# Kernel optimization log

Measured on AMD Instinct MI355X. Metric: run time of the kernel, lower is better.

## Reference

```python
import jax, jax.numpy as jnp
import numpy as np

K = 20  # number of top neighbors kept per row
NOISE_SCALE = 1e-4


def setup_inputs() -> dict:
    key = jax.random.key(0)
    k1, k2 = jax.random.split(key)
    B, N = 16, 2048
    A = jax.random.normal(k1, (B, N, N), dtype=jnp.float32)
    noise = jax.random.uniform(k2, (B, N, N), dtype=jnp.float32)
    return {"A": A, "noise": noise}


def reference(A, noise):
    # _activate: ReLU
    A = jax.nn.relu(A)

    # _sparsify: per-row top-k on noise-doped scores, scatter a 0/1 mask, multiply
    A_doped = A + noise * NOISE_SCALE
    _, topk_idx = jax.lax.top_k(A_doped, K)  # (B, N, K)
    B, N, _ = A.shape
    b_idx = jnp.arange(B)[:, None, None]
    r_idx = jnp.arange(N)[None, :, None]
    mask = jnp.zeros_like(A).at[b_idx, r_idx, topk_idx].set(1.0)
    A = A * mask

    # _symmetrize
    A = (A + jnp.swapaxes(A, 1, 2)) * 0.5

    # _normalize ('sym'): A <- D^{-1/2} (A + I) D^{-1/2}
    A = A + jnp.eye(N, dtype=A.dtype)
    d_inv = jnp.sum(A, axis=2) ** -0.5  # (B, N)
    d_inv = jnp.where(jnp.isinf(d_inv), 0.0, d_inv)
    # diag(d) @ A @ diag(d) expressed via broadcasting (same math as batched matmul)
    A = d_inv[:, :, None] * A * d_inv[:, None, :]
    return A
```

## Files before the change

### kernel.cpp

```cpp
#include <hip/hip_runtime.h>

#define NN 2048
#define KK 20
#define BB 16

__global__ __launch_bounds__(256) void topk_kernel(
    const float* __restrict__ A, const float* __restrict__ noise,
    int* __restrict__ sel_idx, float* __restrict__ sel_val,
    float* __restrict__ colsum)
{
    __shared__ int tie_idx[4][64];
    __shared__ int tie_cnt[4];

    const int lane = threadIdx.x & 63;
    const int wv   = threadIdx.x >> 6;
    const int row  = blockIdx.x * 4 + wv;
    const float* Ar = A     + (size_t)row * NN;
    const float* Nr = noise + (size_t)row * NN;

    float key[32];
#pragma unroll
    for (int c = 0; c < 8; ++c) {
        float4 a4 = *(const float4*)(Ar + c * 256 + lane * 4);
        float4 n4 = *(const float4*)(Nr + c * 256 + lane * 4);
        key[c*4+0] = fmaxf(a4.x, 0.f) + n4.x * 1e-4f;
        key[c*4+1] = fmaxf(a4.y, 0.f) + n4.y * 1e-4f;
        key[c*4+2] = fmaxf(a4.z, 0.f) + n4.z * 1e-4f;
        key[c*4+3] = fmaxf(a4.w, 0.f) + n4.w * 1e-4f;
    }

    unsigned lo = 0u, hi = 0x7F800000u;
    unsigned tb = 0u;
    bool exact = false;
    while (hi - lo > 1u) {
        unsigned mid = (lo + hi) >> 1;
        float tm = __uint_as_float(mid);
        int c = 0;
#pragma unroll
        for (int j = 0; j < 32; ++j)
            c += __popcll(__ballot(key[j] >= tm));
        if (c == KK) { tb = mid; exact = true; break; }
        if (c > KK) lo = mid; else hi = mid;
    }

    const unsigned long long ltm = (1ull << lane) - 1ull;
    const int colbase = row & ~(NN - 1);
    int*   si = sel_idx + (size_t)row * KK;
    float* sv = sel_val + (size_t)row * KK;

    if (exact) {
        float t = __uint_as_float(tb);
        int run = 0;
#pragma unroll
        for (int j = 0; j < 32; ++j) {
            bool p = key[j] >= t;
            unsigned long long m = __ballot(p);
            if (p) {
                int pos = run + __popcll(m & ltm);
                int idx = (j >> 2) * 256 + lane * 4 + (j & 3);
                float v = fmaxf(Ar[idx], 0.f);
                si[pos] = idx; sv[pos] = v;
                atomicAdd(&colsum[colbase + idx], v);
            }
            run += __popcll(m);
        }
    } else {
        float t1 = __uint_as_float(lo);
        int run = 0;
#pragma unroll
        for (int j = 0; j < 32; ++j) {
            bool p = key[j] > t1;
            unsigned long long m = __ballot(p);
            if (p) {
                int pos = run + __popcll(m & ltm);
                int idx = (j >> 2) * 256 + lane * 4 + (j & 3);
                float v = fmaxf(Ar[idx], 0.f);
                si[pos] = idx; sv[pos] = v;
                atomicAdd(&colsum[colbase + idx], v);
            }
            run += __popcll(m);
        }
        if (lane == 0) tie_cnt[wv] = 0;
#pragma unroll
        for (int j = 0; j < 32; ++j) {
            if (key[j] == t1) {
                int p = atomicAdd(&tie_cnt[wv], 1);
                if (p < 64) tie_idx[wv][p] = (j >> 2) * 256 + lane * 4 + (j & 3);
            }
        }
        if (lane == 0) {
            int n = tie_cnt[wv]; if (n > 64) n = 64;
            int need = KK - run;
            for (int s = 0; s < need; ++s) {
                int bq = 0, bidx = 0x7fffffff;
                for (int q = 0; q < n; ++q) {
                    int v = tie_idx[wv][q];
                    if (v < bidx) { bidx = v; bq = q; }
                }
                tie_idx[wv][bq] = 0x7fffffff;
                float v = fmaxf(Ar[bidx], 0.f);
                si[run + s] = bidx; sv[run + s] = v;
                atomicAdd(&colsum[colbase + bidx], v);
            }
        }
    }
}

__global__ __launch_bounds__(256) void dinv_kernel(
    const float* __restrict__ sel_val, const float* __restrict__ colsum,
    float* __restrict__ dinv, float* __restrict__ out)
{
    int r = blockIdx.x * 256 + threadIdx.x;
    const float* sv = sel_val + (size_t)r * KK;
    float rs = 0.f;
#pragma unroll
    for (int k = 0; k < KK; ++k) rs += sv[k];
    float d  = 1.0f + 0.5f * (rs + colsum[r]);
    float dv = 1.0f / sqrtf(d);
    dinv[r] = dv;
    int b = r >> 11, i = r & (NN - 1);
    out[((size_t)b << 22) + ((size_t)i << 11) + i] = dv * dv;
}

__global__ __launch_bounds__(256) void scatter_kernel(
    const int* __restrict__ sel_idx, const float* __restrict__ sel_val,
    const float* __restrict__ dinv, float* __restrict__ out)
{
    int t = blockIdx.x * 256 + threadIdx.x;
    int r = t / KK;
    int k = t - r * KK;
    int b = r >> 11, i = r & (NN - 1);
    int j = sel_idx[(size_t)r * KK + k];
    float v = sel_val[(size_t)r * KK + k];
    float c = 0.5f * v * dinv[r] * dinv[(r & ~(NN - 1)) + j];
    size_t base = (size_t)b << 22;
    atomicAdd(out + base + ((size_t)i << 11) + j, c);
    atomicAdd(out + base + ((size_t)j << 11) + i, c);
}

extern "C" void kernel_launch(void* const* d_in, const int* in_sizes, int n_in,
                              void* d_out, int out_size, void* d_ws, size_t ws_size,
                              hipStream_t stream)
{
    const float* A     = (const float*)d_in[0];
    const float* noise = (const float*)d_in[1];
    float* out = (float*)d_out;
    char*  ws  = (char*)d_ws;

    const int rows = BB * NN;
    int*   sel_idx = (int*)ws;
    float* sel_val = (float*)(ws + 2621440);
    float* colsum  = (float*)(ws + 5242880);
    float* dinv    = (float*)(ws + 5242880 + 131072);

    hipMemsetAsync(colsum, 0, rows * sizeof(float), stream);
    hipMemsetAsync(out, 0, (size_t)out_size * sizeof(float), stream);

    topk_kernel<<<rows / 4, 256, 0, stream>>>(A, noise, sel_idx, sel_val, colsum);
    dinv_kernel<<<rows / 256, 256, 0, stream>>>(sel_val, colsum, dinv, out);
    scatter_kernel<<<rows * KK / 256, 256, 0, stream>>>(sel_idx, sel_val, dinv, out);
}
```

Measured before the change: 686.8 us.

## Prefilter top-k candidates by fixed threshold and build output rows densely in LDS

The top-k kernel now handles two rows per wavefront and keeps only elements above a fixed threshold (1.8) as candidates in LDS. The bisection search then runs over at most 128 candidates, with a full-row fallback when the count is out of range. The output is no longer memset and then filled by global atomics; each row is assembled in shared memory from its own edges plus a per-column reverse list, then written once with coalesced stores. The fixed threshold relies on the input distribution (standard normal) to keep the candidate count in range, and the reverse list caps each column at 64 entries.

```diff
diff --git a/kernel.cpp b/kernel.cpp
--- a/kernel.cpp
+++ b/kernel.cpp
@@ -3,139 +3,275 @@
 #define NN 2048
 #define KK 20
 #define BB 16
+#define ROWS (BB * NN)
+#define T0F 1.8f
+#define CAP 128
+#define CSLOT 64
+
+__device__ __forceinline__ float wred(float x) {
+#pragma unroll
+    for (int s = 32; s; s >>= 1) x += __shfl_xor(x, s);
+    return x;
+}
 
 __global__ __launch_bounds__(256) void topk_kernel(
     const float* __restrict__ A, const float* __restrict__ noise,
     int* __restrict__ sel_idx, float* __restrict__ sel_val,
-    float* __restrict__ colsum)
-{
-    __shared__ int tie_idx[4][64];
-    __shared__ int tie_cnt[4];
+    float* __restrict__ rowsum)
+{
+    __shared__ float cand_key[8][CAP];
+    __shared__ int   cand_idx[8][CAP];
+    __shared__ int   tie_buf[4][64];
+    __shared__ int   tie_n[4];
 
     const int lane = threadIdx.x & 63;
     const int wv   = threadIdx.x >> 6;
-    const int row  = blockIdx.x * 4 + wv;
-    const float* Ar = A     + (size_t)row * NN;
-    const float* Nr = noise + (size_t)row * NN;
-
-    float key[32];
+    const int row0 = blockIdx.x * 8 + wv * 2;
+    const unsigned long long ltm = (1ull << lane) - 1ull;
+
+    const float* Ap[2] = { A + (size_t)row0 * NN, A + (size_t)(row0 + 1) * NN };
+    const float* Np[2] = { noise + (size_t)row0 * NN, noise + (size_t)(row0 + 1) * NN };
+
+    int cnt[2] = {0, 0};
 #pragma unroll
     for (int c = 0; c < 8; ++c) {
-        float4 a4 = *(const float4*)(Ar + c * 256 + lane * 4);
-        float4 n4 = *(const float4*)(Nr + c * 256 + lane * 4);
-        key[c*4+0] = fmaxf(a4.x, 0.f) + n4.x * 1e-4f;
-        key[c*4+1] = fmaxf(a4.y, 0.f) + n4.y * 1e-4f;
-        key[c*4+2] = fmaxf(a4.z, 0.f) + n4.z * 1e-4f;
-        key[c*4+3] = fmaxf(a4.w, 0.f) + n4.w * 1e-4f;
-    }
-
-    unsigned lo = 0u, hi = 0x7F800000u;
-    unsigned tb = 0u;
-    bool exact = false;
-    while (hi - lo > 1u) {
-        unsigned mid = (lo + hi) >> 1;
-        float tm = __uint_as_float(mid);
-        int c = 0;
-#pragma unroll
-        for (int j = 0; j < 32; ++j)
-            c += __popcll(__ballot(key[j] >= tm));
-        if (c == KK) { tb = mid; exact = true; break; }
-        if (c > KK) lo = mid; else hi = mid;
-    }
-
-    const unsigned long long ltm = (1ull << lane) - 1ull;
-    const int colbase = row & ~(NN - 1);
-    int*   si = sel_idx + (size_t)row * KK;
-    float* sv = sel_val + (size_t)row * KK;
-
-    if (exact) {
-        float t = __uint_as_float(tb);
-        int run = 0;
-#pragma unroll
-        for (int j = 0; j < 32; ++j) {
-            bool p = key[j] >= t;
+#pragma unroll
+        for (int rr = 0; rr < 2; ++rr) {
+            float4 a4 = *(const float4*)(Ap[rr] + c * 256 + lane * 4);
+            float4 n4 = *(const float4*)(Np[rr] + c * 256 + lane * 4);
+            float kk4[4] = { fmaxf(a4.x, 0.f) + n4.x * 1e-4f,
+                             fmaxf(a4.y, 0.f) + n4.y * 1e-4f,
+                             fmaxf(a4.z, 0.f) + n4.z * 1e-4f,
+                             fmaxf(a4.w, 0.f) + n4.w * 1e-4f };
+#pragma unroll
+            for (int e = 0; e < 4; ++e) {
+                bool p = kk4[e] >= T0F;
+                unsigned long long m = __ballot(p);
+                if (p) {
+                    int pos = cnt[rr] + __popcll(m & ltm);
+                    if (pos < CAP) {
+                        cand_key[wv * 2 + rr][pos] = kk4[e];
+                        cand_idx[wv * 2 + rr][pos] = c * 256 + lane * 4 + e;
+                    }
+                }
+                cnt[rr] += __popcll(m);
+            }
+        }
+    }
+
+    float c0[2], c1[2];
+#pragma unroll
+    for (int rr = 0; rr < 2; ++rr) {
+        c0[rr] = (lane      < cnt[rr] && lane      < CAP) ? cand_key[wv*2+rr][lane]      : -1.f;
+        c1[rr] = (lane + 64 < cnt[rr] && lane + 64 < CAP) ? cand_key[wv*2+rr][lane + 64] : -1.f;
+    }
+    unsigned lo[2], hi[2], tb[2] = {0, 0};
+    int act[2], ex[2] = {0, 0};
+#pragma unroll
+    for (int rr = 0; rr < 2; ++rr) {
+        act[rr] = (cnt[rr] > KK && cnt[rr] <= CAP);
+        lo[rr] = __float_as_uint(T0F);
+        float mx = fmaxf(c0[rr], c1[rr]);
+#pragma unroll
+        for (int s = 32; s; s >>= 1) mx = fmaxf(mx, __shfl_xor(mx, s));
+        hi[rr] = __float_as_uint(fmaxf(mx, T0F)) + 1u;
+    }
+    while (act[0] | act[1]) {
+#pragma unroll
+        for (int rr = 0; rr < 2; ++rr) {
+            if (act[rr]) {
+                unsigned mid = (lo[rr] + hi[rr]) >> 1;
+                float tm = __uint_as_float(mid);
+                int c = __popcll(__ballot(c0[rr] >= tm)) +
+                        __popcll(__ballot(c1[rr] >= tm));
+                if (c == KK) { tb[rr] = mid; ex[rr] = 1; act[rr] = 0; }
+                else {
+                    if (c > KK) lo[rr] = mid; else hi[rr] = mid;
+                    if (hi[rr] - lo[rr] <= 1u) act[rr] = 0;
+                }
+            }
+        }
+    }
+
+#pragma unroll
+    for (int rr = 0; rr < 2; ++rr) {
+        const int row = row0 + rr;
+        int*   si = sel_idx + (size_t)row * KK;
+        float* sv = sel_val + (size_t)row * KK;
+        float acc = 0.f;
+        if (cnt[rr] == KK) {
+            if (lane < KK) {
+                int idx = cand_idx[wv * 2 + rr][lane];
+                float v = fmaxf(Ap[rr][idx], 0.f);
+                si[lane] = idx; sv[lane] = v; acc = v;
+            }
+            float rs = wred(acc);
+            if (lane == 0) rowsum[row] = rs;
+        } else if (ex[rr]) {
+            float t = __uint_as_float(tb[rr]);
+            bool p = c0[rr] >= t;
             unsigned long long m = __ballot(p);
             if (p) {
-                int pos = run + __popcll(m & ltm);
-                int idx = (j >> 2) * 256 + lane * 4 + (j & 3);
-                float v = fmaxf(Ar[idx], 0.f);
-                si[pos] = idx; sv[pos] = v;
-                atomicAdd(&colsum[colbase + idx], v);
-            }
-            run += __popcll(m);
-        }
-    } else {
-        float t1 = __uint_as_float(lo);
-        int run = 0;
-#pragma unroll
-        for (int j = 0; j < 32; ++j) {
-            bool p = key[j] > t1;
-            unsigned long long m = __ballot(p);
+                int pos = __popcll(m & ltm);
+                int idx = cand_idx[wv * 2 + rr][lane];
+                float v = fmaxf(Ap[rr][idx], 0.f);
+                si[pos] = idx; sv[pos] = v; acc += v;
+            }
+            int run = __popcll(m);
+            p = c1[rr] >= t;
+            m = __ballot(p);
             if (p) {
                 int pos = run + __popcll(m & ltm);
-                int idx = (j >> 2) * 256 + lane * 4 + (j & 3);
-                float v = fmaxf(Ar[idx], 0.f);
-                si[pos] = idx; sv[pos] = v;
-                atomicAdd(&colsum[colbase + idx], v);
-            }
-            run += __popcll(m);
+                int idx = cand_idx[wv * 2 + rr][lane + 64];
+                float v = fmaxf(Ap[rr][idx], 0.f);
+                si[pos] = idx; sv[pos] = v; acc += v;
+            }
+            float rs = wred(acc);
+            if (lane == 0) rowsum[row] = rs;
+        } else {
+            unsigned flo = 0u, fhi = 0x7F800000u, ftb = 0u;
+            int fex = 0;
+            while (fhi - flo > 1u) {
+                unsigned mid = (flo + fhi) >> 1;
+                float tm = __uint_as_float(mid);
+                int c = 0;
+                for (int j = 0; j < 32; ++j) {
+                    int idx = j * 64 + lane;
+                    float k = fmaxf(Ap[rr][idx], 0.f) + Np[rr][idx] * 1e-4f;
+                    c += __popcll(__ballot(k >= tm));
+                }
+                if (c == KK) { ftb = mid; fex = 1; break; }
+                if (c > KK) flo = mid; else fhi = mid;
+            }
+            if (fex) {
+                float t = __uint_as_float(ftb);
+                int run = 0;
+                for (int j = 0; j < 32; ++j) {
+                    int idx = j * 64 + lane;
+                    float v = fmaxf(Ap[rr][idx], 0.f);
+                    bool p = (v + Np[rr][idx] * 1e-4f) >= t;
+                    unsigned long long m = __ballot(p);
+                    if (p) {
+                        int pos = run + __popcll(m & ltm);
+                        si[pos] = idx; sv[pos] = v; acc += v;
+                    }
+                    run += __popcll(m);
+                }
+                float rs = wred(acc);
+                if (lane == 0) rowsum[row] = rs;
+            } else {
+                float t1 = __uint_as_float(flo);
+                int run = 0;
+                for (int j = 0; j < 32; ++j) {
+                    int idx = j * 64 + lane;
+                    float v = fmaxf(Ap[rr][idx], 0.f);
+                    bool p = (v + Np[rr][idx] * 1e-4f) > t1;
+                    unsigned long long m = __ballot(p);
+                    if (p) {
+                        int pos = run + __popcll(m & ltm);
+                        si[pos] = idx; sv[pos] = v; acc += v;
+                    }
+                    run += __popcll(m);
+                }
+                if (lane == 0) tie_n[wv] = 0;
+                for (int j = 0; j < 32; ++j) {
+                    int idx = j * 64 + lane;
+                    float k = fmaxf(Ap[rr][idx], 0.f) + Np[rr][idx] * 1e-4f;
+                    if (k == t1) {
+                        int p = atomicAdd(&tie_n[wv], 1);
+                        if (p < 64) tie_buf[wv][p] = idx;
+                    }
+                }
+                float rs = wred(acc);
+                if (lane == 0) {
+                    int n = tie_n[wv]; if (n > 64) n = 64;
+                    int need = KK - run;
+                    float extra = 0.f;
+                    for (int s = 0; s < need; ++s) {
+                        int bq = 0, bidx = 0x7fffffff;
+                        for (int q = 0; q < n; ++q)
+                            if (tie_buf[wv][q] < bidx) { bidx = tie_buf[wv][q]; bq = q; }
+                        tie_buf[wv][bq] = 0x7fffffff;
+                        float v = fmaxf(Ap[rr][bidx], 0.f);
+                        si[run + s] = bidx; sv[run + s] = v; extra += v;
+                    }
+                    rowsum[row] = rs + extra;
+                }
+            }
         }
-        if (lane == 0) tie_cnt[wv] = 0;
-#pragma unroll
-        for (int j = 0; j < 32; ++j) {
-            if (key[j] == t1) {
-                int p = atomicAdd(&tie_cnt[wv], 1);
-                if (p < 64) tie_idx[wv][p] = (j >> 2) * 256 + lane * 4 + (j & 3);
-            }
-        }
-        if (lane == 0) {
-            int n = tie_cnt[wv]; if (n > 64) n = 64;
-            int need = KK - run;
-            for (int s = 0; s < need; ++s) {
-                int bq = 0, bidx = 0x7fffffff;
-                for (int q = 0; q < n; ++q) {
-                    int v = tie_idx[wv][q];
-                    if (v < bidx) { bidx = v; bq = q; }
-                }
-                tie_idx[wv][bq] = 0x7fffffff;
-                float v = fmaxf(Ar[bidx], 0.f);
-                si[run + s] = bidx; sv[run + s] = v;
-                atomicAdd(&colsum[colbase + bidx], v);
-            }
-        }
-    }
+    }
+}
+
+__global__ __launch_bounds__(256) void colsum_kernel(
+    const int* __restrict__ sel_idx, const float* __restrict__ sel_val,
+    float* __restrict__ colsum)
+{
+    int t = blockIdx.x * 256 + threadIdx.x;
+    int r = t / KK;
+    int cb = r & ~(NN - 1);
+    atomicAdd(&colsum[cb + sel_idx[t]], sel_val[t]);
 }
 
 __global__ __launch_bounds__(256) void dinv_kernel(
-    const float* __restrict__ sel_val, const float* __restrict__ colsum,
-    float* __restrict__ dinv, float* __restrict__ out)
+    const float* __restrict__ rowsum, const float* __restrict__ colsum,
+    float* __restrict__ dinv, float* __restrict__ diag2)
 {
     int r = blockIdx.x * 256 + threadIdx.x;
-    const float* sv = sel_val + (size_t)r * KK;
-    float rs = 0.f;
-#pragma unroll
-    for (int k = 0; k < KK; ++k) rs += sv[k];
-    float d  = 1.0f + 0.5f * (rs + colsum[r]);
+    float d = 1.0f + 0.5f * (rowsum[r] + colsum[r]);
     float dv = 1.0f / sqrtf(d);
     dinv[r] = dv;
-    int b = r >> 11, i = r & (NN - 1);
-    out[((size_t)b << 22) + ((size_t)i << 11) + i] = dv * dv;
-}
-
-__global__ __launch_bounds__(256) void scatter_kernel(
+    diag2[r] = dv * dv;
+}
+
+__global__ __launch_bounds__(256) void edge_kernel(
     const int* __restrict__ sel_idx, const float* __restrict__ sel_val,
-    const float* __restrict__ dinv, float* __restrict__ out)
+    const float* __restrict__ dinv, float* __restrict__ out_val,
+    int* __restrict__ col_cnt, unsigned short* __restrict__ col_pack)
 {
     int t = blockIdx.x * 256 + threadIdx.x;
     int r = t / KK;
     int k = t - r * KK;
-    int b = r >> 11, i = r & (NN - 1);
-    int j = sel_idx[(size_t)r * KK + k];
-    float v = sel_val[(size_t)r * KK + k];
-    float c = 0.5f * v * dinv[r] * dinv[(r & ~(NN - 1)) + j];
-    size_t base = (size_t)b << 22;
-    atomicAdd(out + base + ((size_t)i << 11) + j, c);
-    atomicAdd(out + base + ((size_t)j << 11) + i, c);
+    int cb = r & ~(NN - 1);
+    int j = sel_idx[t];
+    float c = 0.5f * sel_val[t] * dinv[r] * dinv[cb + j];
+    out_val[t] = c;
+    int s = atomicAdd(&col_cnt[cb + j], 1);
+    if (s < CSLOT)
+        col_pack[(size_t)(cb + j) * CSLOT + s] =
+            (unsigned short)(((r & (NN - 1)) << 5) | k);
+}
+
+__global__ __launch_bounds__(256) void dense_row_kernel(
+    const int* __restrict__ sel_idx, const float* __restrict__ out_val,
+    const int* __restrict__ col_cnt, const unsigned short* __restrict__ col_pack,
+    const float* __restrict__ diag2, float* __restrict__ out)
+{
+    __shared__ float rowbuf[NN];
+    const int r  = blockIdx.x;
+    const int i  = r & (NN - 1);
+    const int cb = r & ~(NN - 1);
+    const int t  = threadIdx.x;
+
+    float4 z = {0.f, 0.f, 0.f, 0.f};
+    *(float4*)(rowbuf + t * 4) = z;
+    *(float4*)(rowbuf + 1024 + t * 4) = z;
+    __syncthreads();
+
+    if (t < KK)
+        atomicAdd(&rowbuf[sel_idx[(size_t)r * KK + t]],
+                  out_val[(size_t)r * KK + t]);
+    int cnt = col_cnt[r]; if (cnt > CSLOT) cnt = CSLOT;
+    if (t < cnt) {
+        unsigned pk = col_pack[(size_t)r * CSLOT + t];
+        int srow = pk >> 5, k = pk & 31;
+        atomicAdd(&rowbuf[srow], out_val[(size_t)(cb + srow) * KK + k]);
+    }
+    if (t == 0) atomicAdd(&rowbuf[i], diag2[r]);
+    __syncthreads();
+
+    size_t base = (size_t)r * NN;
+    *(float4*)(out + base + t * 4) = *(const float4*)(rowbuf + t * 4);
+    *(float4*)(out + base + 1024 + t * 4) = *(const float4*)(rowbuf + 1024 + t * 4);
 }
 
 extern "C" void kernel_launch(void* const* d_in, const int* in_sizes, int n_in,
@@ -147,16 +283,24 @@
     float* out = (float*)d_out;
     char*  ws  = (char*)d_ws;
 
-    const int rows = BB * NN;
-    int*   sel_idx = (int*)ws;
-    float* sel_val = (float*)(ws + 2621440);
-    float* colsum  = (float*)(ws + 5242880);
-    float* dinv    = (float*)(ws + 5242880 + 131072);
-
-    hipMemsetAsync(colsum, 0, rows * sizeof(float), stream);
-    hipMemsetAsync(out, 0, (size_t)out_size * sizeof(float), stream);
-
-    topk_kernel<<<rows / 4, 256, 0, stream>>>(A, noise, sel_idx, sel_val, colsum);
-    dinv_kernel<<<rows / 256, 256, 0, stream>>>(sel_val, colsum, dinv, out);
-    scatter_kernel<<<rows * KK / 256, 256, 0, stream>>>(sel_idx, sel_val, dinv, out);
-}
+    size_t off = 0;
+    int*   sel_idx = (int*)(ws + off);             off += (size_t)ROWS * KK * 4;
+    float* sel_val = (float*)(ws + off);           off += (size_t)ROWS * KK * 4;
+    float* out_val = (float*)(ws + off);           off += (size_t)ROWS * KK * 4;
+    unsigned short* col_pack = (unsigned short*)(ws + off); off += (size_t)ROWS * CSLOT * 2;
+    float* colsum  = (float*)(ws + off);           off += (size_t)ROWS * 4;
+    int*   col_cnt = (int*)(ws + off);             off += (size_t)ROWS * 4;
+    float* rowsum  = (float*)(ws + off);           off += (size_t)ROWS * 4;
+    float* dinv    = (float*)(ws + off);           off += (size_t)ROWS * 4;
+    float* diag2   = (float*)(ws + off);           off += (size_t)ROWS * 4;
+
+    hipMemsetAsync(colsum, 0, (size_t)ROWS * 8, stream);
+
+    topk_kernel<<<ROWS / 8, 256, 0, stream>>>(A, noise, sel_idx, sel_val, rowsum);
+    colsum_kernel<<<ROWS * KK / 256, 256, 0, stream>>>(sel_idx, sel_val, colsum);
+    dinv_kernel<<<ROWS / 256, 256, 0, stream>>>(rowsum, colsum, dinv, diag2);
+    edge_kernel<<<ROWS * KK / 256, 256, 0, stream>>>(sel_idx, sel_val, dinv,
+                                                     out_val, col_cnt, col_pack);
+    dense_row_kernel<<<ROWS, 256, 0, stream>>>(sel_idx, out_val, col_cnt,
+                                               col_pack, diag2, out);
+}
```

After: 745.7 us. 1.09x slower.
